# Optimization experiments

Measured on AMD Instinct MI355X. Metric: run time of the kernel, lower is better.

Reference implementation:

```python
import math
import jax, jax.numpy as jnp
import numpy as np

B, S, D, H = 2, 2048, 1024, 16
HD = D // H  # 64
EPS = 1e-5


def _layernorm(x, g, b):
    mu = jnp.mean(x, axis=-1, keepdims=True)
    var = jnp.mean(jnp.square(x - mu), axis=-1, keepdims=True)
    return (x - mu) * jax.lax.rsqrt(var + EPS) * g + b


def setup_inputs() -> dict:
    key = jax.random.key(0)
    ks = jax.random.split(key, 16)
    s_attn = 1.0 / math.sqrt(D)
    s_mlp = 1.0 / math.sqrt(4 * D)
    return {
        "hidden_states": jax.random.normal(ks[0], (B, S, D), jnp.float32),
        # MHA params (torch Linear convention: y = x @ W.T + b)
        "Wqkv": jax.random.normal(ks[1], (3 * D, D), jnp.float32) * s_attn,
        "bqkv": jax.random.normal(ks[2], (3 * D,), jnp.float32) * s_attn,
        "Wout": jax.random.normal(ks[3], (D, D), jnp.float32) * s_attn,
        "bout": jax.random.normal(ks[4], (D,), jnp.float32) * s_attn,
        # LayerNorms
        "g1": jnp.ones((D,), jnp.float32),
        "b1": jnp.zeros((D,), jnp.float32),
        "g2": jnp.ones((D,), jnp.float32),
        "b2": jnp.zeros((D,), jnp.float32),
        # MLP (hidden = 4*D, activation = tanh)
        "W1": jax.random.normal(ks[5], (4 * D, D), jnp.float32) * s_attn,
        "bfc1": jax.random.normal(ks[6], (4 * D,), jnp.float32) * s_attn,
        "W2": jax.random.normal(ks[7], (D, 4 * D), jnp.float32) * s_mlp,
        "bfc2": jax.random.normal(ks[8], (D,), jnp.float32) * s_mlp,
    }


def _mha(x, Wqkv, bqkv, Wout, bout):
    # qkv: (B,S,3,H,hd)
    qkv = (x @ Wqkv.T + bqkv).reshape(B, S, 3, H, HD)
    q, k, v = qkv[:, :, 0], qkv[:, :, 1], qkv[:, :, 2]
    # NOTE: source einsum 'bshd,btjd->bsht' contracts over k's head axis j,
    # so each query head attends against sum-over-heads of K (and of V).
    k_sum = k.sum(axis=2)  # (B,S,hd)
    v_sum = v.sum(axis=2)  # (B,S,hd)
    scale = 1.0 / math.sqrt(HD)
    scores = jnp.einsum('bshd,btd->bsht', q, k_sum) * scale  # (B,S,H,S)
    causal = jnp.triu(jnp.ones((S, S), bool), k=1)  # True above diagonal
    scores = jnp.where(causal[None, :, None, :], -jnp.inf, scores)
    attn = jax.nn.softmax(scores, axis=-1)
    out = jnp.einsum('bsht,btd->bshd', attn, v_sum).reshape(B, S, D)
    return out @ Wout.T + bout


def reference(hidden_states, Wqkv, bqkv, Wout, bout, g1, b1, g2, b2, W1, bfc1, W2, bfc2):
    # eval mode: dropouts and stochastic-depth are identity
    residual = hidden_states
    h = _layernorm(residual, g1, b1)
    h = _mha(h, Wqkv, bqkv, Wout, bout)
    residual = h + residual
    h = _layernorm(residual, g2, b2)
    h = jnp.tanh(h @ W1.T + bfc1) @ W2.T + bfc2
    return (h, residual)
```

## Files before the change

kernel.cpp:

```cpp
#include <hip/hip_runtime.h>
#include <hip/hip_bf16.h>

typedef __attribute__((ext_vector_type(8))) short s16x8;
typedef __attribute__((ext_vector_type(4))) float f32x4;
typedef __hip_bfloat16 bf16_t;

__device__ __forceinline__ void gload_lds16(const void* g, void* l) {
  __builtin_amdgcn_global_load_lds(
      (__attribute__((address_space(1))) void*)(g),
      (__attribute__((address_space(3))) void*)(l), 16, 0, 0);
}

__device__ __forceinline__ unsigned cvt_pk_bf16(float lo, float hi) {
  unsigned r;
  asm("v_cvt_pk_bf16_f32 %0, %1, %2" : "=v"(r) : "v"(lo), "v"(hi));
  return r;
}

__device__ __forceinline__ float fast_tanh(float x) {
  float t = exp2f(x * 2.885390082f);
  return 1.0f - 2.0f * __builtin_amdgcn_rcpf(t + 1.0f);
}

__global__ void cast_all_k(const float* __restrict__ Wqkv, const float* __restrict__ Wout,
                           const float* __restrict__ W1, const float* __restrict__ W2,
                           bf16_t* __restrict__ Wqkv_bf, bf16_t* __restrict__ Wout_bf,
                           bf16_t* __restrict__ W1_bf, bf16_t* __restrict__ W2_bf) {
  int c = blockIdx.x * 256 + threadIdx.x;
  const float* src; bf16_t* dst; int off;
  if (c < 131072)      { src = Wqkv; dst = Wqkv_bf; off = c; }
  else if (c < 262144) { src = Wout; dst = Wout_bf; off = c - 131072; }
  else if (c < 786432) { src = W1;   dst = W1_bf;   off = c - 262144; }
  else                 { src = W2;   dst = W2_bf;   off = c - 786432; }
  int i = off * 8;
  float4 a = *(const float4*)(src + i);
  float4 b = *(const float4*)(src + i + 4);
  union { bf16_t h[8]; s16x8 v; } u;
  u.h[0] = __float2bfloat16(a.x); u.h[1] = __float2bfloat16(a.y);
  u.h[2] = __float2bfloat16(a.z); u.h[3] = __float2bfloat16(a.w);
  u.h[4] = __float2bfloat16(b.x); u.h[5] = __float2bfloat16(b.y);
  u.h[6] = __float2bfloat16(b.z); u.h[7] = __float2bfloat16(b.w);
  *(s16x8*)(dst + i) = u.v;
}

__global__ void reduce_kv_k(const float* __restrict__ Wqkv, bf16_t* __restrict__ Wred) {
  int d   = blockIdx.x & 63;
  int isv = blockIdx.x >> 6;
  int col = threadIdx.x * 4;
  const float* base = Wqkv + (size_t)(1024 + isv * 1024 + d) * 1024 + col;
  float4 s = {0.f, 0.f, 0.f, 0.f};
#pragma unroll
  for (int h = 0; h < 16; ++h) {
    float4 t = *(const float4*)(base + (size_t)h * 64 * 1024);
    s.x += t.x; s.y += t.y; s.z += t.z; s.w += t.w;
  }
  union { bf16_t h[4]; uint2 u; } o;
  o.h[0] = __float2bfloat16(s.x); o.h[1] = __float2bfloat16(s.y);
  o.h[2] = __float2bfloat16(s.z); o.h[3] = __float2bfloat16(s.w);
  *(uint2*)(Wred + (size_t)(isv * 64 + d) * 1024 + col) = o.u;
}

__global__ void bias_prep_k(const float* __restrict__ bqkv, float* __restrict__ br) {
  int i = blockIdx.x * 256 + threadIdx.x;
  if (i >= 1152) return;
  if (i < 1024) { br[i] = bqkv[i]; return; }
  int d = i - 1024;
  int off = (d < 64) ? (1024 + d) : (2048 + (d - 64));
  float s = 0.f;
#pragma unroll
  for (int h = 0; h < 16; ++h) s += bqkv[off + h * 64];
  br[i] = s;
}

__global__ __launch_bounds__(256) void ln_cast_k(const float* __restrict__ x,
                                                 const float* __restrict__ g,
                                                 const float* __restrict__ bb,
                                                 bf16_t* __restrict__ y) {
  int row = blockIdx.x, tid = threadIdx.x;
  float4 v = *(const float4*)(x + (size_t)row * 1024 + tid * 4);
  float s = v.x + v.y + v.z + v.w;
  float q = v.x * v.x + v.y * v.y + v.z * v.z + v.w * v.w;
#pragma unroll
  for (int off = 1; off < 64; off <<= 1) {
    s += __shfl_xor(s, off, 64);
    q += __shfl_xor(q, off, 64);
  }
  __shared__ float ss[4], qq[4];
  int wave = tid >> 6, lane = tid & 63;
  if (lane == 0) { ss[wave] = s; qq[wave] = q; }
  __syncthreads();
  s = ss[0] + ss[1] + ss[2] + ss[3];
  q = qq[0] + qq[1] + qq[2] + qq[3];
  float mu  = s * (1.0f / 1024.0f);
  float var = q * (1.0f / 1024.0f) - mu * mu;
  float rstd = rsqrtf(var + 1e-5f);
  float4 gg = *(const float4*)(g + tid * 4);
  float4 bv = *(const float4*)(bb + tid * 4);
  union { bf16_t h[4]; uint2 u; } o;
  o.h[0] = __float2bfloat16((v.x - mu) * rstd * gg.x + bv.x);
  o.h[1] = __float2bfloat16((v.y - mu) * rstd * gg.y + bv.y);
  o.h[2] = __float2bfloat16((v.z - mu) * rstd * gg.z + bv.z);
  o.h[3] = __float2bfloat16((v.w - mu) * rstd * gg.w + bv.w);
  *(uint2*)(y + (size_t)row * 1024 + tid * 4) = o.u;
}

template <int EPI>
__global__ __launch_bounds__(512) void gemm256(
    const bf16_t* __restrict__ A, const bf16_t* __restrict__ Bw,
    const float* __restrict__ bias, void* __restrict__ out0,
    int M, int N, int K, int Kslice) {
  __shared__ __align__(16) bf16_t As[2 * 16384];
  __shared__ __align__(16) bf16_t Bs[2 * 16384];
  const int tid  = threadIdx.x;
  const int lane = tid & 63;
  const int wave = tid >> 6;
  const int l15 = lane & 15, lg = lane >> 4;
  const int wm = wave >> 2, wn = wave & 3;

  const unsigned nx = gridDim.x, ny = gridDim.y;
  unsigned fid = (blockIdx.z * ny + blockIdx.y) * nx + blockIdx.x;
  const unsigned nwg = nx * ny * gridDim.z;
  fid = (fid & 7) * (nwg >> 3) + (fid >> 3);
  const unsigned bxu = fid % nx;
  const unsigned rem = fid / nx;
  const unsigned byu = rem % ny;
  const unsigned bzu = rem / ny;
  const int bm = byu * 256, bn = bxu * 256;
  const size_t Kz = (size_t)K;
  const int kstart = bzu * Kslice;

  f32x4 acc[8][4];
#pragma unroll
  for (int f = 0; f < 8; ++f)
#pragma unroll
    for (int g = 0; g < 4; ++g) acc[f][g] = (f32x4){0.f, 0.f, 0.f, 0.f};

  const bf16_t* Ab = A + (size_t)bm * Kz + kstart;
  const bf16_t* Bb = Bw + (size_t)bn * Kz + kstart;

  auto stage = [&](int t, int buf) {
    const int k0 = t * 64;
#pragma unroll
    for (int j = 0; j < 4; ++j) {
      const int c   = j * 512 + tid;
      const int row = c >> 3;
      const int kc  = (c & 7) ^ (row & 7);
      gload_lds16(Ab + (size_t)row * Kz + k0 + kc * 8,
                  As + buf * 16384 + (j * 512 + wave * 64) * 8);
      gload_lds16(Bb + (size_t)row * Kz + k0 + kc * 8,
                  Bs + buf * 16384 + (j * 512 + wave * 64) * 8);
    }
  };

  const int NT = Kslice >> 6;
  stage(0, 0);
  int buf = 0;
  for (int t = 0; t < NT; ++t) {
    asm volatile("s_waitcnt vmcnt(0)" ::: "memory");
    __builtin_amdgcn_s_barrier();
    if (t + 1 < NT) stage(t + 1, buf ^ 1);
#pragma unroll
    for (int h = 0; h < 2; ++h) {
      s16x8 af[8], bfv[4];
#pragma unroll
      for (int f = 0; f < 8; ++f) {
        const int row = wm * 128 + f * 16 + l15;
        af[f] = *(const s16x8*)&As[buf * 16384 + (row * 8 + ((h * 4 + lg) ^ (l15 & 7))) * 8];
      }
#pragma unroll
      for (int g = 0; g < 4; ++g) {
        const int row = wn * 64 + g * 16 + l15;
        bfv[g] = *(const s16x8*)&Bs[buf * 16384 + (row * 8 + ((h * 4 + lg) ^ (l15 & 7))) * 8];
      }
      __builtin_amdgcn_s_setprio(1);
#pragma unroll
      for (int f = 0; f < 8; ++f)
#pragma unroll
        for (int g = 0; g < 4; ++g)
          acc[f][g] = __builtin_amdgcn_mfma_f32_16x16x32_bf16(af[f], bfv[g], acc[f][g], 0, 0, 0);
      __builtin_amdgcn_s_setprio(0);
    }
    buf ^= 1;
  }

#pragma unroll
  for (int f = 0; f < 8; ++f) {
    const int row0 = bm + wm * 128 + f * 16 + lg * 4;
#pragma unroll
    for (int g = 0; g < 4; ++g) {
      const int col = bn + wn * 64 + g * 16 + l15;
      const float bcol = (EPI == 4) ? 0.f : bias[col];
#pragma unroll
      for (int r = 0; r < 4; ++r) {
        const int rw = row0 + r;
        float c = acc[f][g][r] + bcol;
        if constexpr (EPI == 2) {
          ((bf16_t*)out0)[(size_t)rw * N + col] = __float2bfloat16(fast_tanh(c));
        } else {
          ((bf16_t*)out0)[((size_t)bzu * M + rw) * N + col] = __float2bfloat16(c);
        }
      }
    }
  }
}

template <int EPI>
__global__ __launch_bounds__(256) void gemm64(
    const bf16_t* __restrict__ A, const bf16_t* __restrict__ Bw,
    const float* __restrict__ bias, void* __restrict__ out0,
    const float* __restrict__ resid, bf16_t* __restrict__ oks,
    bf16_t* __restrict__ ovt, int M, int N, int K) {
  __shared__ __align__(16) bf16_t As[2 * 64 * 32];
  __shared__ __align__(16) bf16_t Bs[2 * 128 * 32];
  const int tid  = threadIdx.x;
  const int lane = tid & 63;
  const int wave = tid >> 6;
  const int l15 = lane & 15, lg = lane >> 4;
  const int wr = (wave >> 1) * 32, wc = (wave & 1) * 64;
  const int bm = blockIdx.y * 64, bn = blockIdx.x * 128;
  const size_t Kz = (size_t)K;
  const int srow = lane >> 2;
  const int scol = ((lane & 3) ^ ((lane >> 3) & 3)) * 8;

  f32x4 acc[2][4];
#pragma unroll
  for (int m = 0; m < 2; ++m)
#pragma unroll
    for (int n = 0; n < 4; ++n) acc[m][n] = (f32x4){0.f, 0.f, 0.f, 0.f};

  const bf16_t* Ab = A + (size_t)bm * Kz;
  const bf16_t* Bb = Bw + (size_t)bn * Kz;

  auto stage = [&](int t, int buf) {
    const int k0 = t * 32;
    gload_lds16(Ab + (size_t)(wave * 16 + srow) * Kz + k0 + scol, As + buf * 2048 + wave * 512);
#pragma unroll
    for (int j = 0; j < 2; ++j) {
      const int cw = wave * 2 + j;
      gload_lds16(Bb + (size_t)(cw * 16 + srow) * Kz + k0 + scol, Bs + buf * 4096 + cw * 512);
    }
  };

  const int NT = K >> 5;
  const int rdoff = (lg ^ ((l15 >> 1) & 3)) * 8;
  stage(0, 0);
  int buf = 0;
  for (int t = 0; t < NT; ++t) {
    __syncthreads();
    if (t + 1 < NT) stage(t + 1, buf ^ 1);
    s16x8 af[2], bfv[4];
#pragma unroll
    for (int m = 0; m < 2; ++m)
      af[m] = *(const s16x8*)&As[buf * 2048 + (wr + m * 16 + l15) * 32 + rdoff];
#pragma unroll
    for (int n = 0; n < 4; ++n)
      bfv[n] = *(const s16x8*)&Bs[buf * 4096 + (wc + n * 16 + l15) * 32 + rdoff];
#pragma unroll
    for (int m = 0; m < 2; ++m)
#pragma unroll
      for (int n = 0; n < 4; ++n)
        acc[m][n] = __builtin_amdgcn_mfma_f32_16x16x32_bf16(af[m], bfv[n], acc[m][n], 0, 0, 0);
    buf ^= 1;
  }

#pragma unroll
  for (int m = 0; m < 2; ++m) {
    const int row0 = bm + wr + m * 16 + lg * 4;
#pragma unroll
    for (int n = 0; n < 4; ++n) {
      const int col = bn + wc + n * 16 + l15;
      const float bcol = bias[col];
#pragma unroll
      for (int r = 0; r < 4; ++r) {
        const int rw = row0 + r;
        float c = acc[m][n][r] + bcol;
        if constexpr (EPI == 0) {
          if (col < 1024) {
            ((bf16_t*)out0)[(size_t)rw * 1024 + col] =
                __float2bfloat16(c * 0.1803368801f);
          } else if (col < 1088) {
            int d = col - 1024, b = rw >> 11, t = rw & 2047;
            oks[((size_t)(b << 11) + t) * 64 + d] = __float2bfloat16(c);
          } else {
            int d = col - 1088, b = rw >> 11, t = rw & 2047;
            ovt[((size_t)b * 64 + d) * 2048 + t] = __float2bfloat16(c);
          }
        } else {
          ((float*)out0)[(size_t)rw * N + col] = c + resid[(size_t)rw * N + col];
        }
      }
    }
  }
}

__global__ __launch_bounds__(256) void fc2_reduce_k(const bf16_t* __restrict__ p,
                                                    const float* __restrict__ bias,
                                                    float* __restrict__ out) {
  const size_t PL = (size_t)4096 * 1024;
  size_t i = ((size_t)blockIdx.x * 256 + threadIdx.x) * 8;
  float acc[8];
  {
    union { s16x8 v; bf16_t h[8]; } u;
    u.v = *(const s16x8*)(p + i);
#pragma unroll
    for (int j = 0; j < 8; ++j) acc[j] = __bfloat162float(u.h[j]);
  }
#pragma unroll
  for (int z = 1; z < 4; ++z) {
    union { s16x8 v; bf16_t h[8]; } u;
    u.v = *(const s16x8*)(p + z * PL + i);
#pragma unroll
    for (int j = 0; j < 8; ++j) acc[j] += __bfloat162float(u.h[j]);
  }
  const int col = (int)(i & 1023);
#pragma unroll
  for (int j = 0; j < 8; ++j) acc[j] += bias[col + j];
  *(float4*)(out + i)     = (float4){acc[0], acc[1], acc[2], acc[3]};
  *(float4*)(out + i + 4) = (float4){acc[4], acc[5], acc[6], acc[7]};
}


template <bool MASK>
__device__ __forceinline__ void attn_tile(
    int t0, int p, const s16x8 (&qf)[2],
    const bf16_t* __restrict__ Ks, const bf16_t* __restrict__ Vs,
    bf16_t* __restrict__ Pl, int l15, int lg,
    float& m_run, float& l_part, f32x4 (&ao)[4]) {
  const int sw7 = l15 & 7;

  f32x4 sc[4];
#pragma unroll
  for (int n = 0; n < 4; ++n) sc[n] = (f32x4){0.f, 0.f, 0.f, 0.f};
#pragma unroll
  for (int ks2 = 0; ks2 < 2; ++ks2) {
#pragma unroll
    for (int n = 0; n < 4; ++n) {
      s16x8 kf = *(const s16x8*)&Ks[(n * 16 + l15) * 64 + (((ks2 << 2) | lg) ^ sw7) * 8];
      sc[n] = __builtin_amdgcn_mfma_f32_16x16x32_bf16(kf, qf[ks2], sc[n], 0, 0, 0);
    }
  }

  float mx = -1e30f;
#pragma unroll
  for (int n = 0; n < 4; ++n) {
#pragma unroll
    for (int r = 0; r < 4; ++r) {
      float v = sc[n][r];
      if (MASK && (t0 + n * 16 + lg * 4 + r > p)) v = -1e30f;
      sc[n][r] = v;
      mx = fmaxf(mx, v);
    }
  }
  if (__any(mx > m_run + 11.5f)) {
    float mxf = fmaxf(mx, __shfl_xor(mx, 16, 64));
    mxf = fmaxf(mxf, __shfl_xor(mxf, 32, 64));
    float mn = fmaxf(m_run, mxf);
    float alpha = exp2f(m_run - mn);
    m_run = mn;
    l_part *= alpha;
#pragma unroll
    for (int r = 0; r < 4; ++r) {
      float ar = __shfl(alpha, lg * 4 + r, 64);
#pragma unroll
      for (int n2 = 0; n2 < 4; ++n2) ao[n2][r] *= ar;
    }
  }
#pragma unroll
  for (int n = 0; n < 4; ++n) {
    float e0 = exp2f(sc[n][0] - m_run);
    float e1 = exp2f(sc[n][1] - m_run);
    float e2 = exp2f(sc[n][2] - m_run);
    float e3 = exp2f(sc[n][3] - m_run);
    l_part += (e0 + e1) + (e2 + e3);
    uint2 d;
    d.x = cvt_pk_bf16(e0, e1);
    d.y = cvt_pk_bf16(e2, e3);
    *(uint2*)&Pl[l15 * 72 + n * 16 + lg * 4] = d;
  }
#pragma unroll
  for (int ks2 = 0; ks2 < 2; ++ks2) {
    s16x8 pa = *(const s16x8*)&Pl[l15 * 72 + ks2 * 32 + lg * 8];
#pragma unroll
    for (int n2 = 0; n2 < 4; ++n2) {
      s16x8 vf = *(const s16x8*)&Vs[(n2 * 16 + l15) * 64 + (((ks2 << 2) | lg) ^ sw7) * 8];
      ao[n2] = __builtin_amdgcn_mfma_f32_16x16x32_bf16(pa, vf, ao[n2], 0, 0, 0);
    }
  }
}

__global__ __launch_bounds__(512) void attn_k(const bf16_t* __restrict__ q,
                                              const bf16_t* __restrict__ ksp,
                                              const bf16_t* __restrict__ vtp,
                                              bf16_t* __restrict__ o) {
  __shared__ __align__(16) bf16_t Ks[2 * 4096];
  __shared__ __align__(16) bf16_t Vs[2 * 4096];
  __shared__ __align__(16) bf16_t Plds[8][16 * 72];
  const int tid = threadIdx.x, lane = tid & 63, wave = tid >> 6;
  const int l15 = lane & 15, lg = lane >> 4;
  const int bi  = blockIdx.x;
  const int b   = bi >> 8;
  const int grp = b ? (255 - (bi & 255)) : (bi & 255);
  const int pbase = 2040 - 8 * grp;
  const int p = pbase + wave;

  const bf16_t* qb_b = q   + (size_t)b * 32768 * 64;
  const bf16_t* ksb  = ksp + (size_t)b * 2048 * 64;
  const bf16_t* vtb  = vtp + (size_t)b * 64 * 2048;
  bf16_t*       ob   = o   + (size_t)b * 32768 * 64;
  bf16_t* Pl = &Plds[wave][0];

  const int srow = lane >> 3;
  const int scol = lane & 7;
  const int grow = wave * 8 + srow;
  const int gcol = scol ^ (grow & 7);
  const bf16_t* ksrc0 = ksb + (size_t)grow * 64 + gcol * 8;
  const bf16_t* vsrc0 = vtb + (size_t)grow * 2048 + gcol * 8;

  auto stageKV = [&](int t, int buf) {
    const int t0 = t * 64;
    gload_lds16(ksrc0 + (size_t)t0 * 64, Ks + buf * 4096 + wave * 512);
    gload_lds16(vsrc0 + t0, Vs + buf * 4096 + wave * 512);
  };

  s16x8 qf[2];
  {
    const bf16_t* qptr = qb_b + (size_t)(16 * p + l15) * 64;
    qf[0] = *(const s16x8*)(qptr + lg * 8);
    qf[1] = *(const s16x8*)(qptr + 32 + lg * 8);
  }

  float m_run = -1e30f, l_part = 0.f;
  f32x4 ao[4];
#pragma unroll
  for (int n = 0; n < 4; ++n) ao[n] = (f32x4){0.f, 0.f, 0.f, 0.f};

  const int nst = (pbase + 71) >> 6;
  stageKV(0, 0);
  int buf = 0;
  for (int tt = 0; tt < nst; ++tt) {
    asm volatile("s_waitcnt vmcnt(0)" ::: "memory");
    __builtin_amdgcn_s_barrier();
    if (tt + 1 < nst) stageKV(tt + 1, buf ^ 1);
    const int t0 = tt * 64;
    if (t0 <= p) {
      const bf16_t* Kc = Ks + buf * 4096;
      const bf16_t* Vc = Vs + buf * 4096;
      if (t0 + 63 <= p)
        attn_tile<false>(t0, p, qf, Kc, Vc, Pl, l15, lg, m_run, l_part, ao);
      else
        attn_tile<true>(t0, p, qf, Kc, Vc, Pl, l15, lg, m_run, l_part, ao);
    }
    buf ^= 1;
  }

  float l2 = l_part + __shfl_xor(l_part, 16, 64);
  l2 += __shfl_xor(l2, 32, 64);
  float rl[4];
#pragma unroll
  for (int r = 0; r < 4; ++r) rl[r] = 1.0f / __shfl(l2, lg * 4 + r, 64);
#pragma unroll
  for (int n2 = 0; n2 < 4; ++n2) {
#pragma unroll
    for (int r = 0; r < 4; ++r) {
      const int row = 16 * p + lg * 4 + r;
      ob[(size_t)row * 64 + n2 * 16 + l15] = __float2bfloat16(ao[n2][r] * rl[r]);
    }
  }
}

extern "C" void kernel_launch(void* const* d_in, const int* in_sizes, int n_in,
                              void* d_out, int out_size, void* d_ws, size_t ws_size,
                              hipStream_t stream) {
  (void)in_sizes; (void)n_in; (void)out_size; (void)ws_size;
  const float* hidden = (const float*)d_in[0];
  const float* Wqkv   = (const float*)d_in[1];
  const float* bqkv   = (const float*)d_in[2];
  const float* Wout   = (const float*)d_in[3];
  const float* bout   = (const float*)d_in[4];
  const float* g1     = (const float*)d_in[5];
  const float* b1     = (const float*)d_in[6];
  const float* g2     = (const float*)d_in[7];
  const float* b2     = (const float*)d_in[8];
  const float* W1     = (const float*)d_in[9];
  const float* bfc1   = (const float*)d_in[10];
  const float* W2     = (const float*)d_in[11];
  const float* bfc2   = (const float*)d_in[12];

  float* out_h   = (float*)d_out;
  float* out_res = out_h + (size_t)4096 * 1024;

  char* ws = (char*)d_ws;
  auto alloc = [&](size_t bytes) {
    char* p = ws;
    ws += (bytes + 255) & ~(size_t)255;
    return p;
  };
  bf16_t* X1      = (bf16_t*)alloc((size_t)4096 * 1024 * 2);
  bf16_t* Wqkv_bf = (bf16_t*)alloc((size_t)1152 * 1024 * 2);
  float*  bias_r  = (float*)alloc(1152 * 4);
  bf16_t* qb      = (bf16_t*)alloc((size_t)4096 * 1024 * 2);
  bf16_t* ksum    = (bf16_t*)alloc((size_t)2 * 2048 * 64 * 2);
  bf16_t* vT      = (bf16_t*)alloc((size_t)2 * 64 * 2048 * 2);
  bf16_t* Ob      = (bf16_t*)alloc((size_t)4096 * 1024 * 2);
  bf16_t* Wout_bf = (bf16_t*)alloc((size_t)1024 * 1024 * 2);
  bf16_t* X2      = (bf16_t*)alloc((size_t)4096 * 1024 * 2);
  bf16_t* W1_bf   = (bf16_t*)alloc((size_t)4096 * 1024 * 2);
  bf16_t* W2_bf   = (bf16_t*)alloc((size_t)1024 * 4096 * 2);
  bf16_t* H1      = (bf16_t*)alloc((size_t)4096 * 4096 * 2);
  bf16_t* fc2_part = (bf16_t*)d_ws;

  cast_all_k<<<5120, 256, 0, stream>>>(Wqkv, Wout, W1, W2, Wqkv_bf, Wout_bf, W1_bf, W2_bf);
  reduce_kv_k<<<128, 256, 0, stream>>>(Wqkv, Wqkv_bf + (size_t)1024 * 1024);
  bias_prep_k<<<5, 256, 0, stream>>>(bqkv, bias_r);

  ln_cast_k<<<4096, 256, 0, stream>>>(hidden, g1, b1, X1);
  gemm64<0><<<dim3(9, 64), 256, 0, stream>>>(X1, Wqkv_bf, bias_r, qb, nullptr, ksum, vT,
                                             4096, 1152, 1024);
  attn_k<<<512, 512, 0, stream>>>(qb, ksum, vT, Ob);
  gemm64<1><<<dim3(8, 64), 256, 0, stream>>>(Ob, Wout_bf, bout, out_res, hidden, nullptr,
                                             nullptr, 4096, 1024, 1024);
  ln_cast_k<<<4096, 256, 0, stream>>>(out_res, g2, b2, X2);
  gemm256<2><<<dim3(16, 16), 512, 0, stream>>>(X2, W1_bf, bfc1, H1, 4096, 4096, 1024, 1024);
  gemm256<4><<<dim3(4, 16, 4), 512, 0, stream>>>(H1, W2_bf, nullptr, fc2_part,
                                                 4096, 1024, 4096, 1024);
  fc2_reduce_k<<<2048, 256, 0, stream>>>(fc2_part, bfc2, out_h);
}
```

Baseline: 217.7 us.

## Split attention KV range into two halves with a separate combine kernel

Each attention block's key/value tile range is split in two (split-K, flash-decoding style), which doubles the grid to 1024 blocks. Each half writes unnormalized fp32 partial outputs plus running max and sum into scratch buffers reused from H1 and X1. A new combine kernel rescales and merges the two partials and writes the bf16 output. This aims to improve load balance and occupancy for the causal triangle, at the cost of extra fp32 partial traffic and one more launch.

```diff
diff --git a/kernel.cpp b/kernel.cpp
--- a/kernel.cpp
+++ b/kernel.cpp
@@ -388,26 +388,34 @@
   }
 }
 
-__global__ __launch_bounds__(512) void attn_k(const bf16_t* __restrict__ q,
-                                              const bf16_t* __restrict__ ksp,
-                                              const bf16_t* __restrict__ vtp,
-                                              bf16_t* __restrict__ o) {
+__global__ __launch_bounds__(512) void attn_part_k(const bf16_t* __restrict__ q,
+                                                   const bf16_t* __restrict__ ksp,
+                                                   const bf16_t* __restrict__ vtp,
+                                                   float* __restrict__ aoP,
+                                                   float* __restrict__ mlP) {
   __shared__ __align__(16) bf16_t Ks[2 * 4096];
   __shared__ __align__(16) bf16_t Vs[2 * 4096];
   __shared__ __align__(16) bf16_t Plds[8][16 * 72];
   const int tid = threadIdx.x, lane = tid & 63, wave = tid >> 6;
   const int l15 = lane & 15, lg = lane >> 4;
-  const int bi  = blockIdx.x;
-  const int b   = bi >> 8;
-  const int grp = b ? (255 - (bi & 255)) : (bi & 255);
+  const int bi   = blockIdx.x;
+  const int half = bi & 1;
+  const int j    = bi >> 1;
+  const int grp  = j & 255;
+  const int b    = j >> 8;
   const int pbase = 2040 - 8 * grp;
   const int p = pbase + wave;
+  const int plane = half * 2 + b;
 
   const bf16_t* qb_b = q   + (size_t)b * 32768 * 64;
   const bf16_t* ksb  = ksp + (size_t)b * 2048 * 64;
   const bf16_t* vtb  = vtp + (size_t)b * 64 * 2048;
-  bf16_t*       ob   = o   + (size_t)b * 32768 * 64;
   bf16_t* Pl = &Plds[wave][0];
+
+  const int nst = (pbase + 71) >> 6;
+  const int na  = (nst + 1) >> 1;
+  const int lo  = half ? na : 0;
+  const int hi  = half ? nst : na;
 
   const int srow = lane >> 3;
   const int scol = lane & 7;
@@ -434,38 +442,75 @@
 #pragma unroll
   for (int n = 0; n < 4; ++n) ao[n] = (f32x4){0.f, 0.f, 0.f, 0.f};
 
-  const int nst = (pbase + 71) >> 6;
-  stageKV(0, 0);
-  int buf = 0;
-  for (int tt = 0; tt < nst; ++tt) {
-    asm volatile("s_waitcnt vmcnt(0)" ::: "memory");
-    __builtin_amdgcn_s_barrier();
-    if (tt + 1 < nst) stageKV(tt + 1, buf ^ 1);
-    const int t0 = tt * 64;
-    if (t0 <= p) {
-      const bf16_t* Kc = Ks + buf * 4096;
-      const bf16_t* Vc = Vs + buf * 4096;
-      if (t0 + 63 <= p)
-        attn_tile<false>(t0, p, qf, Kc, Vc, Pl, l15, lg, m_run, l_part, ao);
-      else
-        attn_tile<true>(t0, p, qf, Kc, Vc, Pl, l15, lg, m_run, l_part, ao);
-    }
-    buf ^= 1;
+  if (lo < hi) {
+    stageKV(lo, 0);
+    int buf = 0;
+    for (int tt = lo; tt < hi; ++tt) {
+      asm volatile("s_waitcnt vmcnt(0)" ::: "memory");
+      __builtin_amdgcn_s_barrier();
+      if (tt + 1 < hi) stageKV(tt + 1, buf ^ 1);
+      const int t0 = tt * 64;
+      if (t0 <= p) {
+        const bf16_t* Kc = Ks + buf * 4096;
+        const bf16_t* Vc = Vs + buf * 4096;
+        if (t0 + 63 <= p)
+          attn_tile<false>(t0, p, qf, Kc, Vc, Pl, l15, lg, m_run, l_part, ao);
+        else
+          attn_tile<true>(t0, p, qf, Kc, Vc, Pl, l15, lg, m_run, l_part, ao);
+      }
+      buf ^= 1;
+    }
   }
 
   float l2 = l_part + __shfl_xor(l_part, 16, 64);
   l2 += __shfl_xor(l2, 32, 64);
-  float rl[4];
-#pragma unroll
-  for (int r = 0; r < 4; ++r) rl[r] = 1.0f / __shfl(l2, lg * 4 + r, 64);
+
+  float* aop = aoP + ((size_t)plane * 32768 + 16 * p) * 64;
 #pragma unroll
   for (int n2 = 0; n2 < 4; ++n2) {
 #pragma unroll
     for (int r = 0; r < 4; ++r) {
-      const int row = 16 * p + lg * 4 + r;
-      ob[(size_t)row * 64 + n2 * 16 + l15] = __float2bfloat16(ao[n2][r] * rl[r]);
-    }
-  }
+      aop[(size_t)(lg * 4 + r) * 64 + n2 * 16 + l15] = ao[n2][r];
+    }
+  }
+  if (lg == 0) {
+    float2* ml = (float2*)mlP;
+    ml[(size_t)plane * 32768 + p * 16 + l15] = make_float2(m_run, l2);
+  }
+}
+
+__global__ __launch_bounds__(256) void attn_combine_k(const float* __restrict__ aoP,
+                                                      const float* __restrict__ mlP,
+                                                      bf16_t* __restrict__ o) {
+  const int gid = blockIdx.x * 256 + threadIdx.x;
+  const int row = gid >> 3;
+  const int seg = gid & 7;
+  const int b   = row >> 15;
+  const int r15 = row & 32767;
+  const float2* ml = (const float2*)mlP;
+  float2 mA = ml[(size_t)(0 * 2 + b) * 32768 + r15];
+  float2 mB = ml[(size_t)(1 * 2 + b) * 32768 + r15];
+  float ms = fmaxf(mA.x, mB.x);
+  float fA = exp2f(mA.x - ms);
+  float fB = exp2f(mB.x - ms);
+  float li = 1.0f / (mA.y * fA + mB.y * fB);
+  fA *= li; fB *= li;
+  const float* pa = aoP + ((size_t)(0 * 2 + b) * 32768 + r15) * 64 + seg * 8;
+  const float* pb = aoP + ((size_t)(1 * 2 + b) * 32768 + r15) * 64 + seg * 8;
+  float4 a0 = *(const float4*)pa;
+  float4 a1 = *(const float4*)(pa + 4);
+  float4 b0 = *(const float4*)pb;
+  float4 b1 = *(const float4*)(pb + 4);
+  union { bf16_t h[8]; s16x8 v; } u;
+  u.h[0] = __float2bfloat16(a0.x * fA + b0.x * fB);
+  u.h[1] = __float2bfloat16(a0.y * fA + b0.y * fB);
+  u.h[2] = __float2bfloat16(a0.z * fA + b0.z * fB);
+  u.h[3] = __float2bfloat16(a0.w * fA + b0.w * fB);
+  u.h[4] = __float2bfloat16(a1.x * fA + b1.x * fB);
+  u.h[5] = __float2bfloat16(a1.y * fA + b1.y * fB);
+  u.h[6] = __float2bfloat16(a1.z * fA + b1.z * fB);
+  u.h[7] = __float2bfloat16(a1.w * fA + b1.w * fB);
+  *(s16x8*)(o + (size_t)row * 64 + seg * 8) = u.v;
 }
 
 extern "C" void kernel_launch(void* const* d_in, const int* in_sizes, int n_in,
@@ -508,6 +553,8 @@
   bf16_t* W2_bf   = (bf16_t*)alloc((size_t)1024 * 4096 * 2);
   bf16_t* H1      = (bf16_t*)alloc((size_t)4096 * 4096 * 2);
   bf16_t* fc2_part = (bf16_t*)d_ws;
+  float* aoP = (float*)H1;
+  float* mlP = (float*)X1;
 
   cast_all_k<<<5120, 256, 0, stream>>>(Wqkv, Wout, W1, W2, Wqkv_bf, Wout_bf, W1_bf, W2_bf);
   reduce_kv_k<<<128, 256, 0, stream>>>(Wqkv, Wqkv_bf + (size_t)1024 * 1024);
@@ -516,7 +563,8 @@
   ln_cast_k<<<4096, 256, 0, stream>>>(hidden, g1, b1, X1);
   gemm64<0><<<dim3(9, 64), 256, 0, stream>>>(X1, Wqkv_bf, bias_r, qb, nullptr, ksum, vT,
                                              4096, 1152, 1024);
-  attn_k<<<512, 512, 0, stream>>>(qb, ksum, vT, Ob);
+  attn_part_k<<<1024, 512, 0, stream>>>(qb, ksum, vT, aoP, mlP);
+  attn_combine_k<<<2048, 256, 0, stream>>>(aoP, mlP, Ob);
   gemm64<1><<<dim3(8, 64), 256, 0, stream>>>(Ob, Wout_bf, bout, out_res, hidden, nullptr,
                                              nullptr, 4096, 1024, 1024);
   ln_cast_k<<<4096, 256, 0, stream>>>(out_res, g2, b2, X2);
```

New measurement: 213.4 us. 1.02x faster.
